# Kernel tuning notes

Hardware: AMD Instinct MI355X
Metric: run time of the kernel (lower is better)

Reference implementation:

```python
import jax, jax.numpy as jnp
import numpy as np

B, N, PREV, PRED, H = 16, 64, 6, 30, 256
E = N * (N - 1)
BN_EPS = 1e-5


def _mlp(x, W1, b1, W2, b2, gamma, beta):
    # Two-layer ELU MLP with batch norm over flattened (batch*rows) dim.
    h = jax.nn.elu(x @ W1 + b1)
    h = jax.nn.elu(h @ W2 + b2)
    b, n, d = h.shape
    f = h.reshape(b * n, d)
    mu = f.mean(axis=0)
    var = f.var(axis=0)
    f = (f - mu) * jax.lax.rsqrt(var + BN_EPS) * gamma + beta
    return f.reshape(b, n, d)


def setup_inputs() -> dict:
    key = jax.random.key(0)
    ks = jax.random.split(key, 8)
    # fully-connected directed graph without self loops
    recv, send = np.where(~np.eye(N, dtype=bool))  # each [E]
    rel_rec = jnp.broadcast_to(jax.nn.one_hot(jnp.asarray(recv), N)[None], (B, E, N)).astype(jnp.float32)
    rel_send = jnp.broadcast_to(jax.nn.one_hot(jnp.asarray(send), N)[None], (B, E, N)).astype(jnp.float32)

    def xavier(k, shape):
        fan_in, fan_out = shape
        std = np.sqrt(2.0 / (fan_in + fan_out))
        return jax.random.normal(k, shape, jnp.float32) * std

    return {
        "prev_actor_centers": jax.random.normal(ks[0], (B, N, PREV, 2), jnp.float32) * 10.0,
        "rel_rec": rel_rec,
        "rel_send": rel_send,
        "W_traj": xavier(ks[1], (PREV * 2, H)),
        "b_traj": jnp.full((H,), 0.1, jnp.float32),
        "n2e_W1": xavier(ks[2], (2 * H, H)),
        "n2e_b1": jnp.full((H,), 0.1, jnp.float32),
        "n2e_W2": xavier(ks[3], (H, H)),
        "n2e_b2": jnp.full((H,), 0.1, jnp.float32),
        "n2e_gamma": jnp.ones((H,), jnp.float32),
        "n2e_beta": jnp.zeros((H,), jnp.float32),
        "e2n_W1": xavier(ks[4], (2 * H, H)),
        "e2n_b1": jnp.full((H,), 0.1, jnp.float32),
        "e2n_W2": xavier(ks[5], (H, H)),
        "e2n_b2": jnp.full((H,), 0.1, jnp.float32),
        "e2n_gamma": jnp.ones((H,), jnp.float32),
        "e2n_beta": jnp.zeros((H,), jnp.float32),
        "W_fuse": xavier(ks[6], (2 * H, H)),
        "b_fuse": jnp.full((H,), 0.1, jnp.float32),
        "W_pred": xavier(ks[7], (H, PRED * 2)),
        "b_pred": jnp.full((PRED * 2,), 0.1, jnp.float32),
    }


def reference(prev_actor_centers, rel_rec, rel_send,
              W_traj, b_traj,
              n2e_W1, n2e_b1, n2e_W2, n2e_b2, n2e_gamma, n2e_beta,
              e2n_W1, e2n_b1, e2n_W2, e2n_b2, e2n_gamma, e2n_beta,
              W_fuse, b_fuse, W_pred, b_pred):
    b, n, prev, _ = prev_actor_centers.shape
    # relative displacements, first step zero
    diffs = prev_actor_centers[:, :, 1:, :] - prev_actor_centers[:, :, :-1, :]
    rel_pos = jnp.concatenate([jnp.zeros((b, n, 1, 2), prev_actor_centers.dtype), diffs], axis=2)
    rel_pos = rel_pos.reshape(b, n, prev * 2)
    x = rel_pos @ W_traj + b_traj  # [b, n, H] node features

    # node2edge: gather via one-hot relation matmuls
    receivers = jnp.einsum('ben,bnh->beh', rel_rec, x)
    senders = jnp.einsum('ben,bnh->beh', rel_send, x)
    edges = jnp.concatenate([receivers, senders], axis=-1)  # [b, E, 2H]
    e = _mlp(edges, n2e_W1, n2e_b1, n2e_W2, n2e_b2, n2e_gamma, n2e_beta)

    # edge2node: degree-normalized scatter via transposed relation matmuls
    deg_rec = rel_rec.sum(axis=1)  # [b, n]
    deg_rec = deg_rec + (deg_rec == 0).astype(deg_rec.dtype)
    incoming = jnp.einsum('ben,beh->bnh', rel_rec, e) / deg_rec[..., None]
    deg_send = rel_send.sum(axis=1)
    deg_send = deg_send + (deg_send == 0).astype(deg_send.dtype)
    outgoing = jnp.einsum('ben,beh->bnh', rel_send, e) / deg_send[..., None]
    nodes = jnp.concatenate([incoming, outgoing], axis=-1)  # [b, n, 2H]
    m = _mlp(nodes, e2n_W1, e2n_b1, e2n_W2, e2n_b2, e2n_gamma, e2n_beta)

    fused = jnp.concatenate([x, m], axis=-1) @ W_fuse + b_fuse  # [b, n, H]
    rel = fused @ W_pred + b_pred  # [b, n, PRED*2]

    current_loc = prev_actor_centers[:, :, -1, :]  # [b, n, 2]
    current_loc = jnp.broadcast_to(current_loc[:, :, None, :], (b, n, PRED, 2)).reshape(b, n, PRED * 2)
    pos = jnp.cumsum(rel.reshape(b, n, PRED, 2), axis=2).reshape(b, n, PRED * 2) + current_loc
    return (rel, pos)
```

## Files before the change

### kernel.cpp

```cpp
#include <hip/hip_runtime.h>
#include <hip/hip_bf16.h>

#define BB 16
#define NN 64
#define PREVN 6
#define PREDN 30
#define HH 256
#define EE 4032
#define EROWS (BB*EE)
#define NROWS (BB*NN)
#define RSE 32
#define RSM 16

typedef short short8 __attribute__((ext_vector_type(8)));
typedef float f32x4 __attribute__((ext_vector_type(4)));

enum : int {
  OFF_STATS_E = 0,
  OFF_STATS_M = 16384,
  OFF_XRS     = 32768,
  F32_END     = 294912
};
enum : size_t {
  BO_W1TE  = 0,
  BO_W2TE  = 131072,
  BO_W1TN  = 196608,
  BO_W2TN  = 327680,
  BO_WFT   = 393216,
  BO_WPT   = 524288,
  BO_XG    = 540672,
  BO_NODES = 802816,
  BO_H1G   = 1327104,
  BO_M2    = 1589248,
  BO_FG    = 1851392,
  BO_E2    = 2113536
};

__device__ __forceinline__ float eluf(float v) { return v > 0.f ? v : __expf(v) - 1.f; }

__device__ __forceinline__ float xembed(const float* __restrict__ centers,
                                        const float* __restrict__ Wt,
                                        const float* __restrict__ bt,
                                        int rr, int col) {
  const float* c = centers + rr * 12;
  float acc = bt[col];
  #pragma unroll
  for (int t = 0; t < 5; ++t) {
    float dx = c[(t+1)*2 + 0] - c[t*2 + 0];
    float dy = c[(t+1)*2 + 1] - c[t*2 + 1];
    acc += dx * Wt[(2 + 2*t)*HH + col] + dy * Wt[(3 + 2*t)*HH + col];
  }
  return acc;
}

struct PrepArgs {
  const float *centers, *W_traj, *b_traj;
  const float *n2e_W1, *n2e_W2, *e2n_W1, *e2n_W2, *W_fuse, *W_pred;
  float* ws;
  float* inc;
  __hip_bfloat16 *p1e, *p2e, *p1n, *p2n, *pf, *pp, *xg;
};

__global__ __launch_bounds__(256) void k_prep(PrepArgs a) {
  const int bid = blockIdx.x, tid = threadIdx.x;
  if (bid < 264) {
    const float* W; __hip_bfloat16* P; int ksh, t0, pad = 0;
    if (bid < 64)       { W = a.n2e_W1; P = a.p1e; ksh = 4; t0 = bid*4; }
    else if (bid < 96)  { W = a.n2e_W2; P = a.p2e; ksh = 3; t0 = (bid-64)*4; }
    else if (bid < 160) { W = a.e2n_W1; P = a.p1n; ksh = 4; t0 = (bid-96)*4; }
    else if (bid < 192) { W = a.e2n_W2; P = a.p2n; ksh = 3; t0 = (bid-160)*4; }
    else if (bid < 256) { W = a.W_fuse; P = a.pf;  ksh = 4; t0 = (bid-192)*4; }
    else                { W = a.W_pred; P = a.pp;  ksh = 3; t0 = (bid-256)*4; pad = 1; }
    const int l = tid & 63, sub = tid >> 6;
    const int t = t0 + sub;
    const int j = t >> ksh, ks = t & ((1 << ksh) - 1);
    const int m16 = l & 15, q = l >> 4;
    __hip_bfloat16* dst = P + ((size_t)t*64 + l)*8;
    if (!pad) {
      const float* src = W + (size_t)(ks*32 + q*8)*256 + j*16 + m16;
      #pragma unroll
      for (int e = 0; e < 8; ++e)
        dst[e] = __float2bfloat16(src[(size_t)e*256]);
    } else {
      const int col = j*16 + m16;
      #pragma unroll
      for (int e = 0; e < 8; ++e)
        dst[e] = __float2bfloat16(col < 60 ?
                     W[(size_t)(ks*32 + q*8 + e)*60 + col] : 0.f);
    }
  } else if (bid < 360) {
    a.ws[(bid - 264) * 256 + tid] = 0.f;
  } else if (bid < 424) {
    int row0 = (bid - 360) * 16;
    #pragma unroll
    for (int r = 0; r < 16; ++r)
      a.xg[(size_t)(row0 + r)*256 + tid] =
          __float2bfloat16(xembed(a.centers, a.W_traj, a.b_traj, row0 + r, tid));
  } else {
    float* p = a.inc + (size_t)(bid - 424) * 4096;
    #pragma unroll
    for (int i = 0; i < 4; ++i)
      *reinterpret_cast<float4*>(p + (i*256 + tid)*4) = (float4){0.f,0.f,0.f,0.f};
  }
}

__global__ __launch_bounds__(64) void k_xrs2(
    const __hip_bfloat16* __restrict__ xg,
    const __hip_bfloat16* __restrict__ W1P,
    const float* __restrict__ b1,
    __hip_bfloat16* __restrict__ xrs) {
  const int lane = threadIdx.x;
  const int m16 = lane & 15, quad = lane >> 4;
  const int ko = quad * 8;
  const int rt = blockIdx.x >> 3, s = blockIdx.x & 7;
  const int half = s >> 2, j0 = (s & 3) * 64;
  const int jg0 = (s & 3) * 4;
  const int row0 = rt * 16;
  __hip_bfloat16* dst = xrs + (size_t)half * 262144;

  f32x4 acc[4];
  #pragma unroll
  for (int jt = 0; jt < 4; ++jt) {
    float bv = half ? 0.f : b1[j0 + jt*16 + m16];
    acc[jt] = (f32x4){bv, bv, bv, bv};
  }
  #pragma unroll
  for (int ks = 0; ks < 8; ++ks) {
    short8 af = *reinterpret_cast<const short8*>(
        xg + (size_t)(row0 + m16)*256 + ks*32 + ko);
    short8 bf[4];
    #pragma unroll
    for (int jt = 0; jt < 4; ++jt)
      bf[jt] = *reinterpret_cast<const short8*>(
          W1P + (((size_t)(jg0 + jt)*16 + half*8 + ks)*64 + lane)*8);
    #pragma unroll
    for (int jt = 0; jt < 4; ++jt)
      acc[jt] = __builtin_amdgcn_mfma_f32_16x16x32_bf16(af, bf[jt], acc[jt], 0, 0, 0);
  }
  #pragma unroll
  for (int jt = 0; jt < 4; ++jt)
    #pragma unroll
    for (int r = 0; r < 4; ++r)
      dst[(size_t)(row0 + quad*4 + r)*256 + j0 + jt*16 + m16] =
          __float2bfloat16(acc[jt][r]);
}

__global__ __launch_bounds__(256, 4) void k_mlp8(
    const __hip_bfloat16* __restrict__ xrs,
    const __hip_bfloat16* __restrict__ W2P,
    const float* __restrict__ b2,
    __hip_bfloat16* __restrict__ outp,
    float* __restrict__ stats,
    float* __restrict__ incraw) {
  __shared__ alignas(16) __hip_bfloat16 h1s[64][264];
  __shared__ float sst[3][256];
  const int tid = threadIdx.x;
  const int w = tid >> 6, lane = tid & 63;
  const int m16 = lane & 15, quad = lane >> 4;
  const int ko = quad * 8;
  const int blk = blockIdx.x;
  const int bb = blk / 63, lb = blk - bb*63;
  const int n0 = (lb * 64) / 63;
  const int thr = (n0 + 1) * 63 - lb * 64;
  const int colw = w * 64;

  #pragma unroll
  for (int i = 0; i < 3; ++i) sst[i][tid] = 0.f;

  {
    const int rg = tid >> 5;
    const int c8 = (tid & 31) * 8;
    const __hip_bfloat16* xrb = xrs + (size_t)(bb*64 + n0)*256 + c8;
    const __hip_bfloat16* xsb = xrs + 262144 + (size_t)bb*64*256 + c8;
    union { uint4 u; __hip_bfloat16 h[8]; } vr0, vr1;
    vr0.u = *reinterpret_cast<const uint4*>(xrb);
    vr1.u = *reinterpret_cast<const uint4*>(xrb + 256);
    #pragma unroll
    for (int i = 0; i < 8; ++i) {
      int r = rg + i*8;
      int isn1 = (r >= thr) ? 1 : 0;
      int rc = n0 + isn1;
      int jj = lb*64 + r - rc*63;
      int sd = jj + (jj >= rc ? 1 : 0);
      union { uint4 u; __hip_bfloat16 h[8]; } vs, va, o;
      vs.u = *reinterpret_cast<const uint4*>(xsb + (size_t)sd*256);
      va.u = isn1 ? vr1.u : vr0.u;
      #pragma unroll
      for (int j = 0; j < 8; ++j)
        o.h[j] = __float2bfloat16(eluf(__bfloat162float(va.h[j]) +
                                       __bfloat162float(vs.h[j])));
      *reinterpret_cast<uint4*>(&h1s[r][c8]) = o.u;
    }
  }
  __syncthreads();

  f32x4 acc2[4][4];
  #pragma unroll
  for (int jt = 0; jt < 4; ++jt) {
    float bv = b2[colw + jt*16 + m16];
    #pragma unroll
    for (int mt = 0; mt < 4; ++mt) acc2[mt][jt] = (f32x4){bv, bv, bv, bv};
  }
  #pragma unroll
  for (int kt = 0; kt < 4; ++kt) {
    #pragma unroll
    for (int ks = 0; ks < 2; ++ks) {
      const int k0 = kt*64 + ks*32 + ko;
      const int chunk = kt*2 + ks;
      short8 af[4], bf[4];
      #pragma unroll
      for (int jt = 0; jt < 4; ++jt)
        bf[jt] = *reinterpret_cast<const short8*>(
            W2P + (((size_t)(w*4 + jt)*8 + chunk)*64 + lane)*8);
      #pragma unroll
      for (int mt = 0; mt < 4; ++mt)
        af[mt] = *(const short8*)((const char*)h1s +
                     (size_t)(mt*16 + m16)*528 + k0*2);
      #pragma unroll
      for (int mt = 0; mt < 4; ++mt)
        #pragma unroll
        for (int jt = 0; jt < 4; ++jt)
          acc2[mt][jt] = __builtin_amdgcn_mfma_f32_16x16x32_bf16(af[mt], bf[jt],
                                                                 acc2[mt][jt], 0, 0, 0);
    }
  }
  __syncthreads();

  #pragma unroll
  for (int jt = 0; jt < 4; ++jt) {
    float s0 = 0.f, s1 = 0.f, sq = 0.f;
    #pragma unroll
    for (int mt = 0; mt < 4; ++mt)
      #pragma unroll
      for (int r = 0; r < 4; ++r) {
        int row = mt*16 + quad*4 + r;
        float hv = eluf(acc2[mt][jt][r]);
        h1s[row][colw + jt*16 + m16] = __float2bfloat16(hv);
        float t1 = (row >= thr) ? hv : 0.f;
        s1 += t1; s0 += hv - t1;
        sq += hv * hv;
      }
    atomicAdd(&sst[0][colw + jt*16 + m16], s0);
    atomicAdd(&sst[1][colw + jt*16 + m16], s1);
    atomicAdd(&sst[2][colw + jt*16 + m16], sq);
  }
  __syncthreads();

  {
    float* sb = stats + (size_t)(blk & (RSE - 1)) * 512;
    float s0 = sst[0][tid], s1 = sst[1][tid];
    atomicAdd(&sb[tid], s0 + s1);
    atomicAdd(&sb[256 + tid], sst[2][tid]);
    atomicAdd(&incraw[(size_t)(bb*64 + n0)*256 + tid], s0);
    atomicAdd(&incraw[(size_t)(bb*64 + n0 + 1)*256 + tid], s1);
  }
  #pragma unroll
  for (int i = 0; i < 8; ++i) {
    int u = i*256 + tid;
    int r = u >> 5, c = (u & 31) * 8;
    int isn1 = (r >= thr) ? 1 : 0;
    int rc = n0 + isn1;
    int jj = lb*64 + r - rc*63;
    int sd = jj + (jj >= rc ? 1 : 0);
    int jpos = rc - (jj < rc ? 1 : 0);
    *reinterpret_cast<uint4*>(outp + ((size_t)(bb*64 + sd)*63 + jpos)*HH + c) =
        *reinterpret_cast<const uint4*>(&h1s[r][c]);
  }
}

__global__ __launch_bounds__(256) void k_aggS(const __hip_bfloat16* __restrict__ e2,
                                              const float* __restrict__ incraw,
                                              const float* __restrict__ st,
                                              const float* __restrict__ gam,
                                              const float* __restrict__ bet,
                                              __hip_bfloat16* __restrict__ nodes) {
  __shared__ float red[8][256];
  const int bn = blockIdx.x;
  const int tid = threadIdx.x;
  const int c8 = (tid & 31) * 8;
  const int rg = tid >> 5;
  const __hip_bfloat16* base = e2 + (size_t)bn * 63 * HH;
  float s[8] = {0.f,0.f,0.f,0.f,0.f,0.f,0.f,0.f};
  for (int j = rg; j < 63; j += 8) {
    union { uint4 u; __hip_bfloat16 h[8]; } v;
    v.u = *reinterpret_cast<const uint4*>(base + (size_t)j*HH + c8);
    #pragma unroll
    for (int jj = 0; jj < 8; ++jj) s[jj] += __bfloat162float(v.h[jj]);
  }
  #pragma unroll
  for (int jj = 0; jj < 8; jj += 4)
    *reinterpret_cast<float4*>(&red[rg][c8 + jj]) =
        (float4){s[jj], s[jj+1], s[jj+2], s[jj+3]};
  float ssum = 0.f, ssq = 0.f;
  #pragma unroll
  for (int r = 0; r < RSE; ++r) {
    ssum += st[(size_t)r*512 + tid];
    ssq  += st[(size_t)r*512 + 256 + tid];
  }
  __syncthreads();
  float S = 0.f;
  #pragma unroll
  for (int r = 0; r < 8; ++r) S += red[r][tid];
  const float inv = 1.f / (float)EROWS;
  float mean = ssum * inv;
  float var  = fmaxf(ssq * inv - mean*mean, 0.f);
  float a = gam[tid] * rsqrtf(var + 1e-5f);
  float c0 = bet[tid] - mean * a;
  float in_v  = a * (incraw[(size_t)bn*256 + tid] * (1.f/63.f)) + c0;
  float out_v = a * (S * (1.f/63.f)) + c0;
  nodes[(size_t)bn*512 + tid]       = __float2bfloat16(in_v);
  nodes[(size_t)bn*512 + 256 + tid] = __float2bfloat16(out_v);
}

__global__ __launch_bounds__(64) void k_n1(
    const __hip_bfloat16* __restrict__ nodes,
    const __hip_bfloat16* __restrict__ W1P,
    const float* __restrict__ b1,
    __hip_bfloat16* __restrict__ h1g) {
  __shared__ alignas(16) __hip_bfloat16 hls[16][40];
  const int lane = threadIdx.x;
  const int m16 = lane & 15, quad = lane >> 4;
  const int ko = quad * 8;
  const int row0 = (blockIdx.x >> 3) * 16;
  const int jb = blockIdx.x & 7;
  const int j0 = jb * 32;

  f32x4 acc[2];
  #pragma unroll
  for (int jt = 0; jt < 2; ++jt) {
    float bv = b1[j0 + jt*16 + m16];
    acc[jt] = (f32x4){bv, bv, bv, bv};
  }
  #pragma unroll
  for (int ks = 0; ks < 16; ++ks) {
    short8 af = *reinterpret_cast<const short8*>(
        nodes + (size_t)(row0 + m16)*512 + ks*32 + ko);
    short8 bf[2];
    #pragma unroll
    for (int jt = 0; jt < 2; ++jt)
      bf[jt] = *reinterpret_cast<const short8*>(
          W1P + (((size_t)(jb*2 + jt)*16 + ks)*64 + lane)*8);
    #pragma unroll
    for (int jt = 0; jt < 2; ++jt)
      acc[jt] = __builtin_amdgcn_mfma_f32_16x16x32_bf16(af, bf[jt], acc[jt], 0, 0, 0);
  }
  #pragma unroll
  for (int jt = 0; jt < 2; ++jt)
    #pragma unroll
    for (int r = 0; r < 4; ++r)
      hls[quad*4 + r][jt*16 + m16] = __float2bfloat16(eluf(acc[jt][r]));
  {
    int r = lane >> 2, c = (lane & 3) * 8;
    *reinterpret_cast<uint4*>(h1g + (size_t)(row0 + r)*256 + j0 + c) =
        *reinterpret_cast<const uint4*>(&hls[r][c]);
  }
}

__global__ __launch_bounds__(64) void k_n2(
    const __hip_bfloat16* __restrict__ h1g,
    const __hip_bfloat16* __restrict__ W2P,
    const float* __restrict__ b2,
    __hip_bfloat16* __restrict__ m2,
    float* __restrict__ stats) {
  __shared__ alignas(16) __hip_bfloat16 hls[16][40];
  __shared__ float sst[2][32];
  const int lane = threadIdx.x;
  const int m16 = lane & 15, quad = lane >> 4;
  const int ko = quad * 8;
  const int row0 = (blockIdx.x >> 3) * 16;
  const int jb = blockIdx.x & 7;
  const int j0 = jb * 32;

  if (lane < 32) { sst[0][lane] = 0.f; sst[1][lane] = 0.f; }

  f32x4 acc[2];
  #pragma unroll
  for (int jt = 0; jt < 2; ++jt) {
    float bv = b2[j0 + jt*16 + m16];
    acc[jt] = (f32x4){bv, bv, bv, bv};
  }
  #pragma unroll
  for (int ks = 0; ks < 8; ++ks) {
    short8 af = *reinterpret_cast<const short8*>(
        h1g + (size_t)(row0 + m16)*256 + ks*32 + ko);
    short8 bf[2];
    #pragma unroll
    for (int jt = 0; jt < 2; ++jt)
      bf[jt] = *reinterpret_cast<const short8*>(
          W2P + (((size_t)(jb*2 + jt)*8 + ks)*64 + lane)*8);
    #pragma unroll
    for (int jt = 0; jt < 2; ++jt)
      acc[jt] = __builtin_amdgcn_mfma_f32_16x16x32_bf16(af, bf[jt], acc[jt], 0, 0, 0);
  }
  #pragma unroll
  for (int jt = 0; jt < 2; ++jt) {
    float ps = 0.f, pq = 0.f;
    #pragma unroll
    for (int r = 0; r < 4; ++r) {
      float hv = eluf(acc[jt][r]);
      hls[quad*4 + r][jt*16 + m16] = __float2bfloat16(hv);
      ps += hv; pq += hv * hv;
    }
    atomicAdd(&sst[0][jt*16 + m16], ps);
    atomicAdd(&sst[1][jt*16 + m16], pq);
  }
  if (lane < 32) {
    float* sb = stats + (size_t)(blockIdx.x & (RSM - 1)) * 512;
    atomicAdd(&sb[j0 + lane], sst[0][lane]);
    atomicAdd(&sb[256 + j0 + lane], sst[1][lane]);
  }
  {
    int r = lane >> 2, c = (lane & 3) * 8;
    *reinterpret_cast<uint4*>(m2 + (size_t)(row0 + r)*256 + j0 + c) =
        *reinterpret_cast<const uint4*>(&hls[r][c]);
  }
}

__global__ __launch_bounds__(64) void k_hf(
    const __hip_bfloat16* __restrict__ xg,
    const __hip_bfloat16* __restrict__ m2,
    const float* __restrict__ stM,
    const float* __restrict__ gam,
    const float* __restrict__ bet,
    const __hip_bfloat16* __restrict__ WfP,
    const float* __restrict__ bfv,
    __hip_bfloat16* __restrict__ fg) {
  __shared__ alignas(16) __hip_bfloat16 hls[16][40];
  __shared__ float bnA[256], bnC[256];
  const int lane = threadIdx.x;
  const int m16 = lane & 15, quad = lane >> 4;
  const int ko = quad * 8;
  const int row0 = (blockIdx.x >> 3) * 16;
  const int jb = blockIdx.x & 7;
  const int j0 = jb * 32;

  {
    const float inv = 1.f / (float)NROWS;
    #pragma unroll
    for (int j = 0; j < 4; ++j) {
      int k = lane*4 + j;
      float ssum = 0.f, ssq = 0.f;
      #pragma unroll
      for (int r = 0; r < RSM; ++r) {
        ssum += stM[(size_t)r*512 + k];
        ssq  += stM[(size_t)r*512 + 256 + k];
      }
      float mean = ssum * inv;
      float var  = fmaxf(ssq * inv - mean*mean, 0.f);
      float am = gam[k] * rsqrtf(var + 1e-5f);
      bnA[k] = am;
      bnC[k] = bet[k] - mean * am;
    }
  }

  f32x4 acc[2];
  #pragma unroll
  for (int jt = 0; jt < 2; ++jt) {
    float bv = bfv[j0 + jt*16 + m16];
    acc[jt] = (f32x4){bv, bv, bv, bv};
  }
  #pragma unroll
  for (int ks = 0; ks < 16; ++ks) {
    short8 af;
    if (ks < 8) {
      af = *reinterpret_cast<const short8*>(
          xg + (size_t)(row0 + m16)*256 + ks*32 + ko);
    } else {
      int k0 = (ks - 8)*32 + ko;
      union { uint4 u; __hip_bfloat16 h[8]; } v;
      v.u = *reinterpret_cast<const uint4*>(m2 + (size_t)(row0 + m16)*256 + k0);
      union { short8 s8; __hip_bfloat16 h[8]; } o;
      #pragma unroll
      for (int j = 0; j < 8; ++j)
        o.h[j] = __float2bfloat16(bnA[k0+j] * __bfloat162float(v.h[j]) + bnC[k0+j]);
      af = o.s8;
    }
    short8 bf[2];
    #pragma unroll
    for (int jt = 0; jt < 2; ++jt)
      bf[jt] = *reinterpret_cast<const short8*>(
          WfP + (((size_t)(jb*2 + jt)*16 + ks)*64 + lane)*8);
    #pragma unroll
    for (int jt = 0; jt < 2; ++jt)
      acc[jt] = __builtin_amdgcn_mfma_f32_16x16x32_bf16(af, bf[jt], acc[jt], 0, 0, 0);
  }
  #pragma unroll
  for (int jt = 0; jt < 2; ++jt)
    #pragma unroll
    for (int r = 0; r < 4; ++r)
      hls[quad*4 + r][jt*16 + m16] = __float2bfloat16(acc[jt][r]);
  {
    int r = lane >> 2, c = (lane & 3) * 8;
    *reinterpret_cast<uint4*>(fg + (size_t)(row0 + r)*256 + j0 + c) =
        *reinterpret_cast<const uint4*>(&hls[r][c]);
  }
}

__global__ __launch_bounds__(64) void k_pred(
    const __hip_bfloat16* __restrict__ fg,
    const __hip_bfloat16* __restrict__ WpP,
    const float* __restrict__ bp,
    const float* __restrict__ centers,
    float* __restrict__ out) {
  __shared__ float rl[16][68];
  const int lane = threadIdx.x;
  const int m16 = lane & 15, quad = lane >> 4;
  const int ko = quad * 8;
  const int row0 = blockIdx.x * 16;

  f32x4 acc[4];
  #pragma unroll
  for (int jt = 0; jt < 4; ++jt) {
    int c = jt*16 + m16;
    float bv = (c < 60) ? bp[c] : 0.f;
    acc[jt] = (f32x4){bv, bv, bv, bv};
  }
  #pragma unroll
  for (int ks = 0; ks < 8; ++ks) {
    short8 af = *reinterpret_cast<const short8*>(
        fg + (size_t)(row0 + m16)*256 + ks*32 + ko);
    short8 bf[4];
    #pragma unroll
    for (int jt = 0; jt < 4; ++jt)
      bf[jt] = *reinterpret_cast<const short8*>(
          WpP + (((size_t)jt*8 + ks)*64 + lane)*8);
    #pragma unroll
    for (int jt = 0; jt < 4; ++jt)
      acc[jt] = __builtin_amdgcn_mfma_f32_16x16x32_bf16(af, bf[jt], acc[jt], 0, 0, 0);
  }
  #pragma unroll
  for (int jt = 0; jt < 4; ++jt) {
    int c = jt*16 + m16;
    #pragma unroll
    for (int r = 0; r < 4; ++r) {
      int lr = quad*4 + r;
      rl[lr][c] = acc[jt][r];
      if (c < 60) out[(size_t)(row0 + lr)*60 + c] = acc[jt][r];
    }
  }
  if (lane < 32) {
    int lr = lane >> 1, xy = lane & 1;
    int grow = row0 + lr;
    float run = centers[(size_t)(grow*PREVN + 5)*2 + xy];
    #pragma unroll
    for (int p = 0; p < PREDN; ++p) {
      run += rl[lr][2*p + xy];
      out[61440 + (size_t)grow*60 + 2*p + xy] = run;
    }
  }
}

extern "C" void kernel_launch(void* const* d_in, const int* in_sizes, int n_in,
                              void* d_out, int out_size, void* d_ws, size_t ws_size,
                              hipStream_t stream) {
  const float* centers = (const float*)d_in[0];
  float* ws = (float*)d_ws;
  __hip_bfloat16* wb = (__hip_bfloat16*)(ws + F32_END);
  __hip_bfloat16* xrs = (__hip_bfloat16*)(ws + OFF_XRS);
  float* incraw = (float*)(wb + BO_H1G);

  const float* W_traj = (const float*)d_in[3];
  const float* b_traj = (const float*)d_in[4];
  const float* n2e_b1 = (const float*)d_in[6];
  const float* n2e_b2 = (const float*)d_in[8];
  const float* n2e_g  = (const float*)d_in[9];
  const float* n2e_be = (const float*)d_in[10];
  const float* e2n_b1 = (const float*)d_in[12];
  const float* e2n_b2 = (const float*)d_in[14];
  const float* e2n_g  = (const float*)d_in[15];
  const float* e2n_be = (const float*)d_in[16];
  const float* b_fuse = (const float*)d_in[18];
  const float* b_pred = (const float*)d_in[20];

  PrepArgs pa;
  pa.centers = centers; pa.W_traj = W_traj; pa.b_traj = b_traj;
  pa.n2e_W1 = (const float*)d_in[5];  pa.n2e_W2 = (const float*)d_in[7];
  pa.e2n_W1 = (const float*)d_in[11]; pa.e2n_W2 = (const float*)d_in[13];
  pa.W_fuse = (const float*)d_in[17]; pa.W_pred = (const float*)d_in[19];
  pa.ws = ws; pa.inc = incraw;
  pa.p1e = wb + BO_W1TE; pa.p2e = wb + BO_W2TE;
  pa.p1n = wb + BO_W1TN; pa.p2n = wb + BO_W2TN;
  pa.pf = wb + BO_WFT;   pa.pp = wb + BO_WPT;
  pa.xg = wb + BO_XG;

  k_prep<<<488, 256, 0, stream>>>(pa);
  k_xrs2<<<512, 64, 0, stream>>>(wb + BO_XG, wb + BO_W1TE, n2e_b1, xrs);
  k_mlp8<<<EROWS/64, 256, 0, stream>>>(xrs, wb + BO_W2TE, n2e_b2, wb + BO_E2,
                                       ws + OFF_STATS_E, incraw);
  k_aggS<<<NROWS, 256, 0, stream>>>(wb + BO_E2, incraw, ws + OFF_STATS_E,
                                    n2e_g, n2e_be, wb + BO_NODES);
  k_n1<<<512, 64, 0, stream>>>(wb + BO_NODES, wb + BO_W1TN, e2n_b1, wb + BO_H1G);
  k_n2<<<512, 64, 0, stream>>>(wb + BO_H1G, wb + BO_W2TN, e2n_b2, wb + BO_M2,
                               ws + OFF_STATS_M);
  k_hf<<<512, 64, 0, stream>>>(wb + BO_XG, wb + BO_M2, ws + OFF_STATS_M,
                               e2n_g, e2n_be, wb + BO_WFT, b_fuse, wb + BO_FG);
  k_pred<<<64, 64, 0, stream>>>(wb + BO_FG, wb + BO_WPT, b_pred, centers,
                                (float*)d_out);
}
```

Before: 182.6 us.

## Fuse node-side kernels and trajectory embedding, transpose weights via shared memory

Merges the trajectory embedding into the first edge-projection kernel, fuses the two node-MLP layers into one kernel, and fuses the fuse and prediction layers into one, going from eight launches to five. Weight packing now goes through a shared-memory tile so global reads are coalesced and packed stores are vectorized. The goal is to cut launch overhead and global round trips for the intermediates. The cost is that the fused node kernels run on only 64 blocks, which lowers parallelism on a GPU with many compute units.

New measurement: 188.3 us. 1.03x slower.

```diff
diff --git a/kernel.cpp b/kernel.cpp
--- a/kernel.cpp
+++ b/kernel.cpp
@@ -32,7 +32,6 @@
   BO_NODES = 802816,
   BO_H1G   = 1327104,
   BO_M2    = 1589248,
-  BO_FG    = 1851392,
   BO_E2    = 2113536
 };
 
@@ -54,94 +53,114 @@
 }
 
 struct PrepArgs {
-  const float *centers, *W_traj, *b_traj;
   const float *n2e_W1, *n2e_W2, *e2n_W1, *e2n_W2, *W_fuse, *W_pred;
   float* ws;
   float* inc;
-  __hip_bfloat16 *p1e, *p2e, *p1n, *p2n, *pf, *pp, *xg;
+  __hip_bfloat16 *p1e, *p2e, *p1n, *p2n, *pf, *pp;
 };
 
 __global__ __launch_bounds__(256) void k_prep(PrepArgs a) {
+  __shared__ float t[64][65];
   const int bid = blockIdx.x, tid = threadIdx.x;
-  if (bid < 264) {
-    const float* W; __hip_bfloat16* P; int ksh, t0, pad = 0;
-    if (bid < 64)       { W = a.n2e_W1; P = a.p1e; ksh = 4; t0 = bid*4; }
-    else if (bid < 96)  { W = a.n2e_W2; P = a.p2e; ksh = 3; t0 = (bid-64)*4; }
-    else if (bid < 160) { W = a.e2n_W1; P = a.p1n; ksh = 4; t0 = (bid-96)*4; }
-    else if (bid < 192) { W = a.e2n_W2; P = a.p2n; ksh = 3; t0 = (bid-160)*4; }
-    else if (bid < 256) { W = a.W_fuse; P = a.pf;  ksh = 4; t0 = (bid-192)*4; }
-    else                { W = a.W_pred; P = a.pp;  ksh = 3; t0 = (bid-256)*4; pad = 1; }
+  if (bid < 128) {
+    const float* W; __hip_bfloat16* P; int K, lb;
+    if (bid < 32)      { W = a.n2e_W1; P = a.p1e; K = 512; lb = bid; }
+    else if (bid < 48) { W = a.n2e_W2; P = a.p2e; K = 256; lb = bid - 32; }
+    else if (bid < 80) { W = a.e2n_W1; P = a.p1n; K = 512; lb = bid - 48; }
+    else if (bid < 96) { W = a.e2n_W2; P = a.p2n; K = 256; lb = bid - 80; }
+    else               { W = a.W_fuse; P = a.pf;  K = 512; lb = bid - 96; }
+    const int KB = K / 64, KC = K / 32;
+    const int k0 = (lb % KB) * 64, n0 = (lb / KB) * 64;
+    const int tx = tid & 63, ty = tid >> 6;
+    #pragma unroll
+    for (int i = 0; i < 16; ++i)
+      t[ty + i*4][tx] = W[(size_t)(k0 + ty + i*4) * 256 + n0 + tx];
+    __syncthreads();
+    const int l = tid & 63, q = l >> 4, m = l & 15;
+    #pragma unroll
+    for (int p = 0; p < 2; ++p) {
+      int tt = (tid >> 6) * 2 + p;
+      int jl = tt >> 1, ksl = tt & 1;
+      union { uint4 u; __hip_bfloat16 h[8]; } o;
+      #pragma unroll
+      for (int e = 0; e < 8; ++e)
+        o.h[e] = __float2bfloat16(t[ksl*32 + q*8 + e][jl*16 + m]);
+      *reinterpret_cast<uint4*>(
+          P + (((size_t)(n0/16 + jl)*KC + (k0/32 + ksl))*64 + l)*8) = o.u;
+    }
+  } else if (bid < 136) {
+    const int t0 = (bid - 128) * 4;
     const int l = tid & 63, sub = tid >> 6;
-    const int t = t0 + sub;
-    const int j = t >> ksh, ks = t & ((1 << ksh) - 1);
+    const int tp = t0 + sub;
+    const int j = tp >> 3, ks = tp & 7;
     const int m16 = l & 15, q = l >> 4;
-    __hip_bfloat16* dst = P + ((size_t)t*64 + l)*8;
-    if (!pad) {
-      const float* src = W + (size_t)(ks*32 + q*8)*256 + j*16 + m16;
-      #pragma unroll
-      for (int e = 0; e < 8; ++e)
-        dst[e] = __float2bfloat16(src[(size_t)e*256]);
-    } else {
-      const int col = j*16 + m16;
-      #pragma unroll
-      for (int e = 0; e < 8; ++e)
-        dst[e] = __float2bfloat16(col < 60 ?
-                     W[(size_t)(ks*32 + q*8 + e)*60 + col] : 0.f);
-    }
-  } else if (bid < 360) {
-    a.ws[(bid - 264) * 256 + tid] = 0.f;
-  } else if (bid < 424) {
-    int row0 = (bid - 360) * 16;
-    #pragma unroll
-    for (int r = 0; r < 16; ++r)
-      a.xg[(size_t)(row0 + r)*256 + tid] =
-          __float2bfloat16(xembed(a.centers, a.W_traj, a.b_traj, row0 + r, tid));
+    __hip_bfloat16* dst = a.pp + ((size_t)tp*64 + l)*8;
+    const int col = j*16 + m16;
+    #pragma unroll
+    for (int e = 0; e < 8; ++e)
+      dst[e] = __float2bfloat16(col < 60 ?
+                   a.W_pred[(size_t)(ks*32 + q*8 + e)*60 + col] : 0.f);
+  } else if (bid < 232) {
+    a.ws[(bid - 136) * 256 + tid] = 0.f;
   } else {
-    float* p = a.inc + (size_t)(bid - 424) * 4096;
+    float* p = a.inc + (size_t)(bid - 232) * 4096;
     #pragma unroll
     for (int i = 0; i < 4; ++i)
       *reinterpret_cast<float4*>(p + (i*256 + tid)*4) = (float4){0.f,0.f,0.f,0.f};
   }
 }
 
-__global__ __launch_bounds__(64) void k_xrs2(
-    const __hip_bfloat16* __restrict__ xg,
+__global__ __launch_bounds__(256) void k_xembxrs(
+    const float* __restrict__ centers,
+    const float* __restrict__ W_traj,
+    const float* __restrict__ b_traj,
     const __hip_bfloat16* __restrict__ W1P,
     const float* __restrict__ b1,
+    __hip_bfloat16* __restrict__ xg,
     __hip_bfloat16* __restrict__ xrs) {
-  const int lane = threadIdx.x;
+  __shared__ alignas(16) __hip_bfloat16 xt[16][264];
+  const int tid = threadIdx.x;
+  const int w = tid >> 6, lane = tid & 63;
   const int m16 = lane & 15, quad = lane >> 4;
   const int ko = quad * 8;
-  const int rt = blockIdx.x >> 3, s = blockIdx.x & 7;
-  const int half = s >> 2, j0 = (s & 3) * 64;
-  const int jg0 = (s & 3) * 4;
-  const int row0 = rt * 16;
+  const int row0 = blockIdx.x * 16;
+
+  #pragma unroll
+  for (int r = 0; r < 16; ++r)
+    xt[r][tid] = __float2bfloat16(xembed(centers, W_traj, b_traj, row0 + r, tid));
+  __syncthreads();
+  #pragma unroll
+  for (int i = 0; i < 2; ++i) {
+    int idx = i*256 + tid;
+    int r = idx >> 5, c = (idx & 31) * 8;
+    *reinterpret_cast<uint4*>(xg + (size_t)(row0 + r)*256 + c) =
+        *reinterpret_cast<const uint4*>(&xt[r][c]);
+  }
+
+  const int half = w >> 1;
+  const int jg0 = (w & 1) * 8;
   __hip_bfloat16* dst = xrs + (size_t)half * 262144;
-
-  f32x4 acc[4];
-  #pragma unroll
-  for (int jt = 0; jt < 4; ++jt) {
-    float bv = half ? 0.f : b1[j0 + jt*16 + m16];
+  f32x4 acc[8];
+  #pragma unroll
+  for (int jt = 0; jt < 8; ++jt) {
+    float bv = half ? 0.f : b1[(jg0 + jt)*16 + m16];
     acc[jt] = (f32x4){bv, bv, bv, bv};
   }
   #pragma unroll
   for (int ks = 0; ks < 8; ++ks) {
-    short8 af = *reinterpret_cast<const short8*>(
-        xg + (size_t)(row0 + m16)*256 + ks*32 + ko);
-    short8 bf[4];
-    #pragma unroll
-    for (int jt = 0; jt < 4; ++jt)
-      bf[jt] = *reinterpret_cast<const short8*>(
+    short8 af = *(const short8*)((const char*)xt + (size_t)m16*528 + (ks*32 + ko)*2);
+    #pragma unroll
+    for (int jt = 0; jt < 8; ++jt) {
+      short8 bf = *reinterpret_cast<const short8*>(
           W1P + (((size_t)(jg0 + jt)*16 + half*8 + ks)*64 + lane)*8);
-    #pragma unroll
-    for (int jt = 0; jt < 4; ++jt)
-      acc[jt] = __builtin_amdgcn_mfma_f32_16x16x32_bf16(af, bf[jt], acc[jt], 0, 0, 0);
-  }
-  #pragma unroll
-  for (int jt = 0; jt < 4; ++jt)
+      acc[jt] = __builtin_amdgcn_mfma_f32_16x16x32_bf16(af, bf, acc[jt], 0, 0, 0);
+    }
+  }
+  #pragma unroll
+  for (int jt = 0; jt < 8; ++jt)
     #pragma unroll
     for (int r = 0; r < 4; ++r)
-      dst[(size_t)(row0 + quad*4 + r)*256 + j0 + jt*16 + m16] =
+      dst[(size_t)(row0 + quad*4 + r)*256 + (jg0 + jt)*16 + m16] =
           __float2bfloat16(acc[jt][r]);
 }
 
@@ -312,111 +331,97 @@
   nodes[(size_t)bn*512 + 256 + tid] = __float2bfloat16(out_v);
 }
 
-__global__ __launch_bounds__(64) void k_n1(
+__global__ __launch_bounds__(256) void k_nmlp(
     const __hip_bfloat16* __restrict__ nodes,
     const __hip_bfloat16* __restrict__ W1P,
     const float* __restrict__ b1,
-    __hip_bfloat16* __restrict__ h1g) {
-  __shared__ alignas(16) __hip_bfloat16 hls[16][40];
-  const int lane = threadIdx.x;
-  const int m16 = lane & 15, quad = lane >> 4;
-  const int ko = quad * 8;
-  const int row0 = (blockIdx.x >> 3) * 16;
-  const int jb = blockIdx.x & 7;
-  const int j0 = jb * 32;
-
-  f32x4 acc[2];
-  #pragma unroll
-  for (int jt = 0; jt < 2; ++jt) {
-    float bv = b1[j0 + jt*16 + m16];
-    acc[jt] = (f32x4){bv, bv, bv, bv};
-  }
-  #pragma unroll
-  for (int ks = 0; ks < 16; ++ks) {
-    short8 af = *reinterpret_cast<const short8*>(
-        nodes + (size_t)(row0 + m16)*512 + ks*32 + ko);
-    short8 bf[2];
-    #pragma unroll
-    for (int jt = 0; jt < 2; ++jt)
-      bf[jt] = *reinterpret_cast<const short8*>(
-          W1P + (((size_t)(jb*2 + jt)*16 + ks)*64 + lane)*8);
-    #pragma unroll
-    for (int jt = 0; jt < 2; ++jt)
-      acc[jt] = __builtin_amdgcn_mfma_f32_16x16x32_bf16(af, bf[jt], acc[jt], 0, 0, 0);
-  }
-  #pragma unroll
-  for (int jt = 0; jt < 2; ++jt)
-    #pragma unroll
-    for (int r = 0; r < 4; ++r)
-      hls[quad*4 + r][jt*16 + m16] = __float2bfloat16(eluf(acc[jt][r]));
-  {
-    int r = lane >> 2, c = (lane & 3) * 8;
-    *reinterpret_cast<uint4*>(h1g + (size_t)(row0 + r)*256 + j0 + c) =
-        *reinterpret_cast<const uint4*>(&hls[r][c]);
-  }
-}
-
-__global__ __launch_bounds__(64) void k_n2(
-    const __hip_bfloat16* __restrict__ h1g,
     const __hip_bfloat16* __restrict__ W2P,
     const float* __restrict__ b2,
     __hip_bfloat16* __restrict__ m2,
     float* __restrict__ stats) {
-  __shared__ alignas(16) __hip_bfloat16 hls[16][40];
-  __shared__ float sst[2][32];
-  const int lane = threadIdx.x;
+  __shared__ alignas(16) __hip_bfloat16 h1[16][264];
+  __shared__ alignas(16) __hip_bfloat16 m2s[16][264];
+  __shared__ float sst[2][256];
+  const int tid = threadIdx.x;
+  const int w = tid >> 6, lane = tid & 63;
   const int m16 = lane & 15, quad = lane >> 4;
   const int ko = quad * 8;
-  const int row0 = (blockIdx.x >> 3) * 16;
-  const int jb = blockIdx.x & 7;
-  const int j0 = jb * 32;
-
-  if (lane < 32) { sst[0][lane] = 0.f; sst[1][lane] = 0.f; }
-
-  f32x4 acc[2];
-  #pragma unroll
-  for (int jt = 0; jt < 2; ++jt) {
-    float bv = b2[j0 + jt*16 + m16];
-    acc[jt] = (f32x4){bv, bv, bv, bv};
-  }
-  #pragma unroll
-  for (int ks = 0; ks < 8; ++ks) {
-    short8 af = *reinterpret_cast<const short8*>(
-        h1g + (size_t)(row0 + m16)*256 + ks*32 + ko);
-    short8 bf[2];
-    #pragma unroll
-    for (int jt = 0; jt < 2; ++jt)
-      bf[jt] = *reinterpret_cast<const short8*>(
-          W2P + (((size_t)(jb*2 + jt)*8 + ks)*64 + lane)*8);
-    #pragma unroll
-    for (int jt = 0; jt < 2; ++jt)
-      acc[jt] = __builtin_amdgcn_mfma_f32_16x16x32_bf16(af, bf[jt], acc[jt], 0, 0, 0);
-  }
-  #pragma unroll
-  for (int jt = 0; jt < 2; ++jt) {
-    float ps = 0.f, pq = 0.f;
-    #pragma unroll
-    for (int r = 0; r < 4; ++r) {
-      float hv = eluf(acc[jt][r]);
-      hls[quad*4 + r][jt*16 + m16] = __float2bfloat16(hv);
-      ps += hv; pq += hv * hv;
-    }
-    atomicAdd(&sst[0][jt*16 + m16], ps);
-    atomicAdd(&sst[1][jt*16 + m16], pq);
-  }
-  if (lane < 32) {
+  const int row0 = blockIdx.x * 16;
+  sst[0][tid] = 0.f; sst[1][tid] = 0.f;
+
+  {
+    f32x4 acc[4];
+    #pragma unroll
+    for (int jt = 0; jt < 4; ++jt) {
+      float bv = b1[w*64 + jt*16 + m16];
+      acc[jt] = (f32x4){bv, bv, bv, bv};
+    }
+    #pragma unroll
+    for (int ks = 0; ks < 16; ++ks) {
+      short8 af = *reinterpret_cast<const short8*>(
+          nodes + (size_t)(row0 + m16)*512 + ks*32 + ko);
+      #pragma unroll
+      for (int jt = 0; jt < 4; ++jt) {
+        short8 bf = *reinterpret_cast<const short8*>(
+            W1P + (((size_t)(w*4 + jt)*16 + ks)*64 + lane)*8);
+        acc[jt] = __builtin_amdgcn_mfma_f32_16x16x32_bf16(af, bf, acc[jt], 0, 0, 0);
+      }
+    }
+    #pragma unroll
+    for (int jt = 0; jt < 4; ++jt)
+      #pragma unroll
+      for (int r = 0; r < 4; ++r)
+        h1[quad*4 + r][w*64 + jt*16 + m16] = __float2bfloat16(eluf(acc[jt][r]));
+  }
+  __syncthreads();
+
+  {
+    f32x4 acc[4];
+    #pragma unroll
+    for (int jt = 0; jt < 4; ++jt) {
+      float bv = b2[w*64 + jt*16 + m16];
+      acc[jt] = (f32x4){bv, bv, bv, bv};
+    }
+    #pragma unroll
+    for (int ks = 0; ks < 8; ++ks) {
+      short8 af = *(const short8*)((const char*)h1 +
+                      (size_t)m16*528 + (ks*32 + ko)*2);
+      #pragma unroll
+      for (int jt = 0; jt < 4; ++jt) {
+        short8 bf = *reinterpret_cast<const short8*>(
+            W2P + (((size_t)(w*4 + jt)*8 + ks)*64 + lane)*8);
+        acc[jt] = __builtin_amdgcn_mfma_f32_16x16x32_bf16(af, bf, acc[jt], 0, 0, 0);
+      }
+    }
+    #pragma unroll
+    for (int jt = 0; jt < 4; ++jt) {
+      float ps = 0.f, pq = 0.f;
+      #pragma unroll
+      for (int r = 0; r < 4; ++r) {
+        float hv = eluf(acc[jt][r]);
+        m2s[quad*4 + r][w*64 + jt*16 + m16] = __float2bfloat16(hv);
+        ps += hv; pq += hv * hv;
+      }
+      atomicAdd(&sst[0][w*64 + jt*16 + m16], ps);
+      atomicAdd(&sst[1][w*64 + jt*16 + m16], pq);
+    }
+  }
+  __syncthreads();
+  {
     float* sb = stats + (size_t)(blockIdx.x & (RSM - 1)) * 512;
-    atomicAdd(&sb[j0 + lane], sst[0][lane]);
-    atomicAdd(&sb[256 + j0 + lane], sst[1][lane]);
-  }
-  {
-    int r = lane >> 2, c = (lane & 3) * 8;
-    *reinterpret_cast<uint4*>(m2 + (size_t)(row0 + r)*256 + j0 + c) =
-        *reinterpret_cast<const uint4*>(&hls[r][c]);
-  }
-}
-
-__global__ __launch_bounds__(64) void k_hf(
+    atomicAdd(&sb[tid], sst[0][tid]);
+    atomicAdd(&sb[256 + tid], sst[1][tid]);
+  }
+  #pragma unroll
+  for (int i = 0; i < 2; ++i) {
+    int idx = i*256 + tid;
+    int r = idx >> 5, c = (idx & 31) * 8;
+    *reinterpret_cast<uint4*>(m2 + (size_t)(row0 + r)*256 + c) =
+        *reinterpret_cast<const uint4*>(&m2s[r][c]);
+  }
+}
+
+__global__ __launch_bounds__(256) void k_hfp(
     const __hip_bfloat16* __restrict__ xg,
     const __hip_bfloat16* __restrict__ m2,
     const float* __restrict__ stM,
@@ -424,122 +429,95 @@
     const float* __restrict__ bet,
     const __hip_bfloat16* __restrict__ WfP,
     const float* __restrict__ bfv,
-    __hip_bfloat16* __restrict__ fg) {
-  __shared__ alignas(16) __hip_bfloat16 hls[16][40];
-  __shared__ float bnA[256], bnC[256];
-  const int lane = threadIdx.x;
-  const int m16 = lane & 15, quad = lane >> 4;
-  const int ko = quad * 8;
-  const int row0 = (blockIdx.x >> 3) * 16;
-  const int jb = blockIdx.x & 7;
-  const int j0 = jb * 32;
-
-  {
-    const float inv = 1.f / (float)NROWS;
-    #pragma unroll
-    for (int j = 0; j < 4; ++j) {
-      int k = lane*4 + j;
-      float ssum = 0.f, ssq = 0.f;
-      #pragma unroll
-      for (int r = 0; r < RSM; ++r) {
-        ssum += stM[(size_t)r*512 + k];
-        ssq  += stM[(size_t)r*512 + 256 + k];
-      }
-      float mean = ssum * inv;
-      float var  = fmaxf(ssq * inv - mean*mean, 0.f);
-      float am = gam[k] * rsqrtf(var + 1e-5f);
-      bnA[k] = am;
-      bnC[k] = bet[k] - mean * am;
-    }
-  }
-
-  f32x4 acc[2];
-  #pragma unroll
-  for (int jt = 0; jt < 2; ++jt) {
-    float bv = bfv[j0 + jt*16 + m16];
-    acc[jt] = (f32x4){bv, bv, bv, bv};
-  }
-  #pragma unroll
-  for (int ks = 0; ks < 16; ++ks) {
-    short8 af;
-    if (ks < 8) {
-      af = *reinterpret_cast<const short8*>(
-          xg + (size_t)(row0 + m16)*256 + ks*32 + ko);
-    } else {
-      int k0 = (ks - 8)*32 + ko;
-      union { uint4 u; __hip_bfloat16 h[8]; } v;
-      v.u = *reinterpret_cast<const uint4*>(m2 + (size_t)(row0 + m16)*256 + k0);
-      union { short8 s8; __hip_bfloat16 h[8]; } o;
-      #pragma unroll
-      for (int j = 0; j < 8; ++j)
-        o.h[j] = __float2bfloat16(bnA[k0+j] * __bfloat162float(v.h[j]) + bnC[k0+j]);
-      af = o.s8;
-    }
-    short8 bf[2];
-    #pragma unroll
-    for (int jt = 0; jt < 2; ++jt)
-      bf[jt] = *reinterpret_cast<const short8*>(
-          WfP + (((size_t)(jb*2 + jt)*16 + ks)*64 + lane)*8);
-    #pragma unroll
-    for (int jt = 0; jt < 2; ++jt)
-      acc[jt] = __builtin_amdgcn_mfma_f32_16x16x32_bf16(af, bf[jt], acc[jt], 0, 0, 0);
-  }
-  #pragma unroll
-  for (int jt = 0; jt < 2; ++jt)
-    #pragma unroll
-    for (int r = 0; r < 4; ++r)
-      hls[quad*4 + r][jt*16 + m16] = __float2bfloat16(acc[jt][r]);
-  {
-    int r = lane >> 2, c = (lane & 3) * 8;
-    *reinterpret_cast<uint4*>(fg + (size_t)(row0 + r)*256 + j0 + c) =
-        *reinterpret_cast<const uint4*>(&hls[r][c]);
-  }
-}
-
-__global__ __launch_bounds__(64) void k_pred(
-    const __hip_bfloat16* __restrict__ fg,
     const __hip_bfloat16* __restrict__ WpP,
     const float* __restrict__ bp,
     const float* __restrict__ centers,
     float* __restrict__ out) {
+  __shared__ alignas(16) __hip_bfloat16 fgs[16][264];
+  __shared__ float bnA[256], bnC[256];
   __shared__ float rl[16][68];
-  const int lane = threadIdx.x;
+  const int tid = threadIdx.x;
+  const int w = tid >> 6, lane = tid & 63;
   const int m16 = lane & 15, quad = lane >> 4;
   const int ko = quad * 8;
   const int row0 = blockIdx.x * 16;
 
-  f32x4 acc[4];
-  #pragma unroll
-  for (int jt = 0; jt < 4; ++jt) {
-    int c = jt*16 + m16;
+  {
+    const float inv = 1.f / (float)NROWS;
+    float ssum = 0.f, ssq = 0.f;
+    #pragma unroll
+    for (int r = 0; r < RSM; ++r) {
+      ssum += stM[(size_t)r*512 + tid];
+      ssq  += stM[(size_t)r*512 + 256 + tid];
+    }
+    float mean = ssum * inv;
+    float var  = fmaxf(ssq * inv - mean*mean, 0.f);
+    float am = gam[tid] * rsqrtf(var + 1e-5f);
+    bnA[tid] = am;
+    bnC[tid] = bet[tid] - mean * am;
+  }
+  __syncthreads();
+
+  {
+    f32x4 acc[4];
+    #pragma unroll
+    for (int jt = 0; jt < 4; ++jt) {
+      float bv = bfv[w*64 + jt*16 + m16];
+      acc[jt] = (f32x4){bv, bv, bv, bv};
+    }
+    #pragma unroll
+    for (int ks = 0; ks < 16; ++ks) {
+      short8 af;
+      if (ks < 8) {
+        af = *reinterpret_cast<const short8*>(
+            xg + (size_t)(row0 + m16)*256 + ks*32 + ko);
+      } else {
+        int k0 = (ks - 8)*32 + ko;
+        union { uint4 u; __hip_bfloat16 h[8]; } v;
+        v.u = *reinterpret_cast<const uint4*>(m2 + (size_t)(row0 + m16)*256 + k0);
+        union { short8 s8; __hip_bfloat16 h[8]; } o;
+        #pragma unroll
+        for (int j = 0; j < 8; ++j)
+          o.h[j] = __float2bfloat16(bnA[k0+j] * __bfloat162float(v.h[j]) + bnC[k0+j]);
+        af = o.s8;
+      }
+      #pragma unroll
+      for (int jt = 0; jt < 4; ++jt) {
+        short8 bf = *reinterpret_cast<const short8*>(
+            WfP + (((size_t)(w*4 + jt)*16 + ks)*64 + lane)*8);
+        acc[jt] = __builtin_amdgcn_mfma_f32_16x16x32_bf16(af, bf, acc[jt], 0, 0, 0);
+      }
+    }
+    #pragma unroll
+    for (int jt = 0; jt < 4; ++jt)
+      #pragma unroll
+      for (int r = 0; r < 4; ++r)
+        fgs[quad*4 + r][w*64 + jt*16 + m16] = __float2bfloat16(acc[jt][r]);
+  }
+  __syncthreads();
+
+  {
+    int c = w*16 + m16;
     float bv = (c < 60) ? bp[c] : 0.f;
-    acc[jt] = (f32x4){bv, bv, bv, bv};
-  }
-  #pragma unroll
-  for (int ks = 0; ks < 8; ++ks) {
-    short8 af = *reinterpret_cast<const short8*>(
-        fg + (size_t)(row0 + m16)*256 + ks*32 + ko);
-    short8 bf[4];
-    #pragma unroll
-    for (int jt = 0; jt < 4; ++jt)
-      bf[jt] = *reinterpret_cast<const short8*>(
-          WpP + (((size_t)jt*8 + ks)*64 + lane)*8);
-    #pragma unroll
-    for (int jt = 0; jt < 4; ++jt)
-      acc[jt] = __builtin_amdgcn_mfma_f32_16x16x32_bf16(af, bf[jt], acc[jt], 0, 0, 0);
-  }
-  #pragma unroll
-  for (int jt = 0; jt < 4; ++jt) {
-    int c = jt*16 + m16;
+    f32x4 ap = (f32x4){bv, bv, bv, bv};
+    #pragma unroll
+    for (int ks = 0; ks < 8; ++ks) {
+      short8 af = *(const short8*)((const char*)fgs +
+                      (size_t)m16*528 + (ks*32 + ko)*2);
+      short8 bf = *reinterpret_cast<const short8*>(
+          WpP + (((size_t)w*8 + ks)*64 + lane)*8);
+      ap = __builtin_amdgcn_mfma_f32_16x16x32_bf16(af, bf, ap, 0, 0, 0);
+    }
     #pragma unroll
     for (int r = 0; r < 4; ++r) {
       int lr = quad*4 + r;
-      rl[lr][c] = acc[jt][r];
-      if (c < 60) out[(size_t)(row0 + lr)*60 + c] = acc[jt][r];
-    }
-  }
-  if (lane < 32) {
-    int lr = lane >> 1, xy = lane & 1;
+      rl[lr][c] = ap[r];
+      if (c < 60) out[(size_t)(row0 + lr)*60 + c] = ap[r];
+    }
+  }
+  __syncthreads();
+  if (tid < 32) {
+    int lr = tid >> 1, xy = tid & 1;
     int grow = row0 + lr;
     float run = centers[(size_t)(grow*PREVN + 5)*2 + xy];
     #pragma unroll
@@ -573,7 +551,6 @@
   const float* b_pred = (const float*)d_in[20];
 
   PrepArgs pa;
-  pa.centers = centers; pa.W_traj = W_traj; pa.b_traj = b_traj;
   pa.n2e_W1 = (const float*)d_in[5];  pa.n2e_W2 = (const float*)d_in[7];
   pa.e2n_W1 = (const float*)d_in[11]; pa.e2n_W2 = (const float*)d_in[13];
   pa.W_fuse = (const float*)d_in[17]; pa.W_pred = (const float*)d_in[19];
@@ -581,19 +558,18 @@
   pa.p1e = wb + BO_W1TE; pa.p2e = wb + BO_W2TE;
   pa.p1n = wb + BO_W1TN; pa.p2n = wb + BO_W2TN;
   pa.pf = wb + BO_WFT;   pa.pp = wb + BO_WPT;
-  pa.xg = wb + BO_XG;
-
-  k_prep<<<488, 256, 0, stream>>>(pa);
-  k_xrs2<<<512, 64, 0, stream>>>(wb + BO_XG, wb + BO_W1TE, n2e_b1, xrs);
+
+  k_prep<<<296, 256, 0, stream>>>(pa);
+  k_xembxrs<<<64, 256, 0, stream>>>(centers, W_traj, b_traj,
+                                    wb + BO_W1TE, n2e_b1, wb + BO_XG, xrs);
   k_mlp8<<<EROWS/64, 256, 0, stream>>>(xrs, wb + BO_W2TE, n2e_b2, wb + BO_E2,
                                        ws + OFF_STATS_E, incraw);
   k_aggS<<<NROWS, 256, 0, stream>>>(wb + BO_E2, incraw, ws + OFF_STATS_E,
                                     n2e_g, n2e_be, wb + BO_NODES);
-  k_n1<<<512, 64, 0, stream>>>(wb + BO_NODES, wb + BO_W1TN, e2n_b1, wb + BO_H1G);
-  k_n2<<<512, 64, 0, stream>>>(wb + BO_H1G, wb + BO_W2TN, e2n_b2, wb + BO_M2,
-                               ws + OFF_STATS_M);
-  k_hf<<<512, 64, 0, stream>>>(wb + BO_XG, wb + BO_M2, ws + OFF_STATS_M,
-                               e2n_g, e2n_be, wb + BO_WFT, b_fuse, wb + BO_FG);
-  k_pred<<<64, 64, 0, stream>>>(wb + BO_FG, wb + BO_WPT, b_pred, centers,
-                                (float*)d_out);
-}
+  k_nmlp<<<64, 256, 0, stream>>>(wb + BO_NODES, wb + BO_W1TN, e2n_b1,
+                                 wb + BO_W2TN, e2n_b2, wb + BO_M2,
+                                 ws + OFF_STATS_M);
+  k_hfp<<<64, 256, 0, stream>>>(wb + BO_XG, wb + BO_M2, ws + OFF_STATS_M,
+                                e2n_g, e2n_be, wb + BO_WFT, b_fuse,
+                                wb + BO_WPT, b_pred, centers, (float*)d_out);
+}
```

## Enlarge edge-MLP row tile to 96 rows and reduce stats via wave shuffles

Applied to the files above, without the earlier changes.

The second-layer edge MLP kernel now handles 96 edge rows per block instead of 64, so each block spans up to three receiver nodes. Each loaded W2 fragment feeds six MFMA row tiles instead of four, which cuts weight traffic per row and the block count. The shared-memory atomic stats buffer is replaced by cross-quad shuffle reductions, with direct global atomics issued from one quad. The costs are more accumulator registers, lower occupancy (launch bound 3), and more global atomics per block.

Measured after the change: 174.9 us, median of 2. -4.2%, faster.

```diff
diff --git a/kernel.cpp b/kernel.cpp
--- a/kernel.cpp
+++ b/kernel.cpp
@@ -145,46 +145,43 @@
           __float2bfloat16(acc[jt][r]);
 }
 
-__global__ __launch_bounds__(256, 4) void k_mlp8(
+__global__ __launch_bounds__(256, 3) void k_mlp96(
     const __hip_bfloat16* __restrict__ xrs,
     const __hip_bfloat16* __restrict__ W2P,
     const float* __restrict__ b2,
     __hip_bfloat16* __restrict__ outp,
     float* __restrict__ stats,
     float* __restrict__ incraw) {
-  __shared__ alignas(16) __hip_bfloat16 h1s[64][264];
-  __shared__ float sst[3][256];
+  __shared__ alignas(16) __hip_bfloat16 h1s[96][264];
   const int tid = threadIdx.x;
   const int w = tid >> 6, lane = tid & 63;
   const int m16 = lane & 15, quad = lane >> 4;
   const int ko = quad * 8;
   const int blk = blockIdx.x;
-  const int bb = blk / 63, lb = blk - bb*63;
-  const int n0 = (lb * 64) / 63;
-  const int thr = (n0 + 1) * 63 - lb * 64;
+  const int bb = blk / 42, lb = blk - bb*42;
+  const int n0 = (lb * 96) / 63;
+  const int thr1 = (n0 + 1) * 63 - lb * 96;
+  const int thr2 = thr1 + 63;
   const int colw = w * 64;
-
-  #pragma unroll
-  for (int i = 0; i < 3; ++i) sst[i][tid] = 0.f;
 
   {
     const int rg = tid >> 5;
     const int c8 = (tid & 31) * 8;
     const __hip_bfloat16* xrb = xrs + (size_t)(bb*64 + n0)*256 + c8;
     const __hip_bfloat16* xsb = xrs + 262144 + (size_t)bb*64*256 + c8;
-    union { uint4 u; __hip_bfloat16 h[8]; } vr0, vr1;
+    union { uint4 u; __hip_bfloat16 h[8]; } vr0, vr1, vr2;
     vr0.u = *reinterpret_cast<const uint4*>(xrb);
     vr1.u = *reinterpret_cast<const uint4*>(xrb + 256);
-    #pragma unroll
-    for (int i = 0; i < 8; ++i) {
+    vr2.u = (thr2 < 96) ? *reinterpret_cast<const uint4*>(xrb + 512) : vr0.u;
+    #pragma unroll
+    for (int i = 0; i < 12; ++i) {
       int r = rg + i*8;
-      int isn1 = (r >= thr) ? 1 : 0;
-      int rc = n0 + isn1;
-      int jj = lb*64 + r - rc*63;
+      int rc = n0 + ((r >= thr1) ? 1 : 0) + ((r >= thr2) ? 1 : 0);
+      int jj = lb*96 + r - rc*63;
       int sd = jj + (jj >= rc ? 1 : 0);
       union { uint4 u; __hip_bfloat16 h[8]; } vs, va, o;
       vs.u = *reinterpret_cast<const uint4*>(xsb + (size_t)sd*256);
-      va.u = isn1 ? vr1.u : vr0.u;
+      va.u = (r >= thr2) ? vr2.u : ((r >= thr1) ? vr1.u : vr0.u);
       #pragma unroll
       for (int j = 0; j < 8; ++j)
         o.h[j] = __float2bfloat16(eluf(__bfloat162float(va.h[j]) +
@@ -194,73 +191,72 @@
   }
   __syncthreads();
 
-  f32x4 acc2[4][4];
+  f32x4 acc2[6][4];
   #pragma unroll
   for (int jt = 0; jt < 4; ++jt) {
     float bv = b2[colw + jt*16 + m16];
     #pragma unroll
-    for (int mt = 0; mt < 4; ++mt) acc2[mt][jt] = (f32x4){bv, bv, bv, bv};
-  }
-  #pragma unroll
-  for (int kt = 0; kt < 4; ++kt) {
-    #pragma unroll
-    for (int ks = 0; ks < 2; ++ks) {
-      const int k0 = kt*64 + ks*32 + ko;
-      const int chunk = kt*2 + ks;
-      short8 af[4], bf[4];
+    for (int mt = 0; mt < 6; ++mt) acc2[mt][jt] = (f32x4){bv, bv, bv, bv};
+  }
+  #pragma unroll
+  for (int chunk = 0; chunk < 8; ++chunk) {
+    const int k0 = chunk*32 + ko;
+    short8 af[6], bf[4];
+    #pragma unroll
+    for (int jt = 0; jt < 4; ++jt)
+      bf[jt] = *reinterpret_cast<const short8*>(
+          W2P + (((size_t)(w*4 + jt)*8 + chunk)*64 + lane)*8);
+    #pragma unroll
+    for (int mt = 0; mt < 6; ++mt)
+      af[mt] = *(const short8*)((const char*)h1s +
+                   (size_t)(mt*16 + m16)*528 + k0*2);
+    #pragma unroll
+    for (int mt = 0; mt < 6; ++mt)
       #pragma unroll
       for (int jt = 0; jt < 4; ++jt)
-        bf[jt] = *reinterpret_cast<const short8*>(
-            W2P + (((size_t)(w*4 + jt)*8 + chunk)*64 + lane)*8);
-      #pragma unroll
-      for (int mt = 0; mt < 4; ++mt)
-        af[mt] = *(const short8*)((const char*)h1s +
-                     (size_t)(mt*16 + m16)*528 + k0*2);
-      #pragma unroll
-      for (int mt = 0; mt < 4; ++mt)
-        #pragma unroll
-        for (int jt = 0; jt < 4; ++jt)
-          acc2[mt][jt] = __builtin_amdgcn_mfma_f32_16x16x32_bf16(af[mt], bf[jt],
-                                                                 acc2[mt][jt], 0, 0, 0);
-    }
+        acc2[mt][jt] = __builtin_amdgcn_mfma_f32_16x16x32_bf16(af[mt], bf[jt],
+                                                               acc2[mt][jt], 0, 0, 0);
   }
   __syncthreads();
 
   #pragma unroll
   for (int jt = 0; jt < 4; ++jt) {
-    float s0 = 0.f, s1 = 0.f, sq = 0.f;
-    #pragma unroll
-    for (int mt = 0; mt < 4; ++mt)
+    float s0 = 0.f, s1 = 0.f, s2 = 0.f, sq = 0.f;
+    #pragma unroll
+    for (int mt = 0; mt < 6; ++mt)
       #pragma unroll
       for (int r = 0; r < 4; ++r) {
         int row = mt*16 + quad*4 + r;
         float hv = eluf(acc2[mt][jt][r]);
         h1s[row][colw + jt*16 + m16] = __float2bfloat16(hv);
-        float t1 = (row >= thr) ? hv : 0.f;
-        s1 += t1; s0 += hv - t1;
+        float v2 = (row >= thr2) ? hv : 0.f;
+        float v1 = (row >= thr1) ? hv - v2 : 0.f;
+        s2 += v2; s1 += v1; s0 += hv - v1 - v2;
         sq += hv * hv;
       }
-    atomicAdd(&sst[0][colw + jt*16 + m16], s0);
-    atomicAdd(&sst[1][colw + jt*16 + m16], s1);
-    atomicAdd(&sst[2][colw + jt*16 + m16], sq);
+    s0 += __shfl_xor(s0, 16); s0 += __shfl_xor(s0, 32);
+    s1 += __shfl_xor(s1, 16); s1 += __shfl_xor(s1, 32);
+    s2 += __shfl_xor(s2, 16); s2 += __shfl_xor(s2, 32);
+    sq += __shfl_xor(sq, 16); sq += __shfl_xor(sq, 32);
+    if (quad == 0) {
+      int col = colw + jt*16 + m16;
+      float* sb = stats + (size_t)(blk & (RSE - 1)) * 512;
+      atomicAdd(&sb[col], s0 + s1 + s2);
+      atomicAdd(&sb[256 + col], sq);
+      atomicAdd(&incraw[(size_t)(bb*64 + n0)*256 + col], s0);
+      atomicAdd(&incraw[(size_t)(bb*64 + n0 + 1)*256 + col], s1);
+      if (thr2 < 96)
+        atomicAdd(&incraw[(size_t)(bb*64 + n0 + 2)*256 + col], s2);
+    }
   }
   __syncthreads();
 
-  {
-    float* sb = stats + (size_t)(blk & (RSE - 1)) * 512;
-    float s0 = sst[0][tid], s1 = sst[1][tid];
-    atomicAdd(&sb[tid], s0 + s1);
-    atomicAdd(&sb[256 + tid], sst[2][tid]);
-    atomicAdd(&incraw[(size_t)(bb*64 + n0)*256 + tid], s0);
-    atomicAdd(&incraw[(size_t)(bb*64 + n0 + 1)*256 + tid], s1);
-  }
-  #pragma unroll
-  for (int i = 0; i < 8; ++i) {
+  #pragma unroll
+  for (int i = 0; i < 12; ++i) {
     int u = i*256 + tid;
     int r = u >> 5, c = (u & 31) * 8;
-    int isn1 = (r >= thr) ? 1 : 0;
-    int rc = n0 + isn1;
-    int jj = lb*64 + r - rc*63;
+    int rc = n0 + ((r >= thr1) ? 1 : 0) + ((r >= thr2) ? 1 : 0);
+    int jj = lb*96 + r - rc*63;
     int sd = jj + (jj >= rc ? 1 : 0);
     int jpos = rc - (jj < rc ? 1 : 0);
     *reinterpret_cast<uint4*>(outp + ((size_t)(bb*64 + sd)*63 + jpos)*HH + c) =
@@ -585,8 +581,8 @@
 
   k_prep<<<488, 256, 0, stream>>>(pa);
   k_xrs2<<<512, 64, 0, stream>>>(wb + BO_XG, wb + BO_W1TE, n2e_b1, xrs);
-  k_mlp8<<<EROWS/64, 256, 0, stream>>>(xrs, wb + BO_W2TE, n2e_b2, wb + BO_E2,
-                                       ws + OFF_STATS_E, incraw);
+  k_mlp96<<<EROWS/96, 256, 0, stream>>>(xrs, wb + BO_W2TE, n2e_b2, wb + BO_E2,
+                                        ws + OFF_STATS_E, incraw);
   k_aggS<<<NROWS, 256, 0, stream>>>(wb + BO_E2, incraw, ws + OFF_STATS_E,
                                     n2e_g, n2e_be, wb + BO_NODES);
   k_n1<<<512, 64, 0, stream>>>(wb + BO_NODES, wb + BO_W1TN, e2n_b1, wb + BO_H1G);
```
